# Kernel optimization log

Hardware: AMD Instinct MI355X
Metric: run time of the kernel (lower is better)

The kernel has to match this reference:

```python
import jax, jax.numpy as jnp
import numpy as np

T, M, K, B, H, L, V = 64, 256, 6, 256, 256, 128, 780
E = T * M
PAD = E  # padding slot in hidden buffer = Lorentz origin

def _to_lorentz_np(s):
    t = np.sqrt(1.0 + (s * s).sum(-1, keepdims=True))
    return np.concatenate([t, s], -1).astype(np.float32)

def setup_inputs() -> dict:
    rng = np.random.default_rng(0)
    def make_nei():
        idx = np.full((T, M, K), PAD, np.int64)
        w = np.zeros((T, M, K), np.float32)
        for t in range(T):
            deg = rng.integers(0, K + 1, size=M)
            if t == 0:
                deg[:] = 0  # no messages exist yet
            mask = np.arange(K)[None, :] < deg[:, None]
            cand = rng.integers(0, max(1, t * M), size=(M, K))  # only already-computed slots
            idx[t] = np.where(mask, cand, PAD)
            w[t] = mask.astype(np.float32)
            w[t, deg == 0, 0] = 1.0  # zero-neighbor case -> use origin padding (as in torch code)
        return idx.astype(np.int32), w
    nei_h_idx, nei_h_w = make_nei()
    nei_o_idx, nei_o_w = make_nei()
    return dict(
        wid=jnp.asarray(rng.integers(0, V, size=(T, M)), jnp.int32),
        nei_h_idx=jnp.asarray(nei_h_idx), nei_h_w=jnp.asarray(nei_h_w),
        nei_o_idx=jnp.asarray(nei_o_idx), nei_o_w=jnp.asarray(nei_o_w),
        batch_idx=jnp.asarray(rng.integers(0, B, size=(T, M)), jnp.int32),
        direction=jnp.asarray(rng.integers(0, 2, size=(T, M)), jnp.int32),
        pred_target=jnp.asarray(rng.integers(0, V, size=(T, M)), jnp.int32),
        root_wid=jnp.asarray(rng.integers(0, V, size=(B,)), jnp.int32),
        root_o_idx=jnp.asarray(rng.integers(0, E, size=(B, K)), jnp.int32),
        root_o_w=jnp.ones((B, K), jnp.float32),
        x_tree_vecs=jnp.asarray(_to_lorentz_np(rng.standard_normal((B, L - 1)) * 0.5)),
        embedding=jnp.asarray(_to_lorentz_np(rng.standard_normal((V, H - 1)) * 0.5)),
        W0=jnp.asarray(rng.standard_normal((H, H)) * 0.02, dtype=jnp.float32),
        b0=jnp.zeros((H,), jnp.float32),
        s0=jnp.asarray(np.log(10.0), jnp.float32),
        W1=jnp.asarray(rng.standard_normal((H, 2 * H - 1)) * 0.02, dtype=jnp.float32),
        b1=jnp.zeros((H,), jnp.float32),
        s1=jnp.asarray(np.log(10.0), jnp.float32),
        wcls=jnp.asarray(_to_lorentz_np(rng.standard_normal((V, H + L - 2)) * 0.5)),
        wbias=jnp.zeros((V,), jnp.float32),
        ucls=jnp.asarray(_to_lorentz_np(rng.standard_normal((2, 2 * H + L - 3)) * 0.5)),
        ubias=jnp.zeros((2,), jnp.float32),
    )

def _llinear(x, W, b, scale):
    # LorentzLinear: affine map, then rescale space part so output stays on the hyperboloid
    x = x @ W.T + b
    xs = x[..., 1:]
    time = jax.nn.sigmoid(x[..., :1]) * jnp.exp(scale) + 1.1
    sq = (time * time - 1.0) / jnp.clip((xs * xs).sum(-1, keepdims=True), 1e-8)
    return jnp.concatenate([time, xs * jnp.sqrt(sq)], -1)

def _mid_point(x, w):
    # Lorentz centroid: weighted mean renormalized to the manifold. x: [...,K,d], w: [...,K]
    ave = jnp.einsum('...k,...kd->...d', w, x) / jnp.clip(w.sum(-1, keepdims=True), 1e-8)
    inner = (ave[..., 1:] ** 2).sum(-1, keepdims=True) - ave[..., :1] ** 2  # <ave,ave>_L
    return ave / jnp.sqrt(jnp.clip(-inner, 1e-8))

def _concat(x, y):
    # hyperbolic concat: keep space parts, recompute time (dim = d1+d2-1)
    time = jnp.sqrt(jnp.clip(x[..., :1] ** 2 + y[..., :1] ** 2 - 1.0, 1e-8))
    return jnp.concatenate([time, x[..., 1:], y[..., 1:]], -1)

def _centroid(x, cls_pts, bias):
    # LorentzCentroidDistance logits: 2 + 2*<x, c>_L + bias
    inner = x[..., 1:] @ cls_pts[:, 1:].T - x[..., :1] * cls_pts[None, :, 0]
    return 2.0 + 2.0 * inner + bias

def _ce(scores, tgt):
    lp = jax.nn.log_softmax(scores, -1)
    return -jnp.take_along_axis(lp, tgt[:, None], axis=-1)[:, 0]

def _forward_core(wid, nei_h_idx, nei_h_w, nei_o_idx, nei_o_w, batch_idx, direction,
                  pred_target, root_wid, root_o_idx, root_o_w, x_tree_vecs, embedding,
                  W0, b0, s0, W1, b1, s1, wcls, wbias, ucls, ubias):
    hbuf0 = jnp.zeros((E + 1, H), jnp.float32).at[:, 0].set(1.0)  # all origin; slot E is padding

    def step(carry, xs_t):
        hbuf, t = carry
        wid_t, idx_t, w_t = xs_t
        cur_x = embedding[wid_t]                      # [M,H]
        h_nei = hbuf[idx_t]                           # [M,K,H] gather of prior messages
        h1 = _llinear(h_nei, W0, b0, s0)              # A0
        h1m = _mid_point(h1, w_t)                     # [M,H]
        new_h = _llinear(_concat(cur_x, h1m), W1, b1, s1)  # A1
        hbuf = jax.lax.dynamic_update_slice(hbuf, new_h, (t * M, 0))
        return (hbuf, t + jnp.int32(1)), new_h

    (hbuf, _), new_h = jax.lax.scan(step, (hbuf0, jnp.int32(0)), (wid, nei_h_idx, nei_h_w))
    new_h = new_h.reshape(E, H)
    cur_x = embedding[wid.reshape(E)]
    cur_o = _mid_point(hbuf[nei_o_idx.reshape(E, K)], nei_o_w.reshape(E, K))
    ctx = x_tree_vecs[batch_idx.reshape(E)]

    # word prediction: roots (origin hidden) + forward-direction messages
    origin = jnp.zeros((B, H), jnp.float32).at[:, 0].set(1.0)
    root_scores = _centroid(_concat(origin, x_tree_vecs), wcls, wbias)   # [B,V]
    msg_scores = _centroid(_concat(new_h, ctx), wcls, wbias)             # [E,V]
    pmask = direction.reshape(E).astype(jnp.float32)
    pt = pred_target.reshape(E)
    pred_loss = (_ce(root_scores, root_wid).sum() + (pmask * _ce(msg_scores, pt)).sum()) / B
    pred_hit = ((jnp.argmax(root_scores, -1) == root_wid).astype(jnp.float32).sum()
                + (pmask * (jnp.argmax(msg_scores, -1) == pt).astype(jnp.float32)).sum())
    pred_acc = pred_hit / (B + pmask.sum())

    # stop prediction: every message + final per-tree root entry (target 0)
    stop_h = _concat(_concat(cur_x, cur_o), ctx)                         # [E, 2H+L-2]
    root_o = _mid_point(hbuf[root_o_idx], root_o_w)
    stop_root = _concat(_concat(embedding[root_wid], root_o), x_tree_vecs)
    stop_scores = _centroid(jnp.concatenate([stop_h, stop_root], 0), ucls, ubias)
    stop_tgt = jnp.concatenate([direction.reshape(E), jnp.zeros((B,), jnp.int32)], 0)
    stop_loss = _ce(stop_scores, stop_tgt).sum() / B
    stop_acc = (jnp.argmax(stop_scores, -1) == stop_tgt).astype(jnp.float32).mean()
    return pred_loss, stop_loss, pred_acc, stop_acc

def reference(wid, nei_h_idx, nei_h_w, nei_o_idx, nei_o_w, batch_idx, direction,
              pred_target, root_wid, root_o_idx, root_o_w, x_tree_vecs, embedding,
              W0, b0, s0, W1, b1, s1, wcls, wbias, ucls, ubias):
    return _forward_core(wid, nei_h_idx, nei_h_w, nei_o_idx, nei_o_w, batch_idx, direction,
                         pred_target, root_wid, root_o_idx, root_o_w, x_tree_vecs, embedding,
                         W0, b0, s0, W1, b1, s1, wcls, wbias, ucls, ubias)
```

## Files before the change

### kernel.cpp

```cpp
#include <hip/hip_runtime.h>
#include <math.h>

#define T_ 64
#define M_ 256
#define K_ 6
#define B_ 256
#define H_ 256
#define L_ 128
#define V_ 780
#define E_ (T_*M_)
#define ZD 383
#define UD 638
#define KP 384
#define VP 832
#define TAG_PAD 0x7fffffffu

typedef unsigned short ushort_t;
typedef __attribute__((ext_vector_type(8))) _Float16 half8v;
typedef __attribute__((ext_vector_type(4))) _Float16 half4v;
typedef __attribute__((ext_vector_type(2))) _Float16 half2v;
typedef __attribute__((ext_vector_type(4))) float f32x4v;
typedef unsigned long long u64;


__device__ __forceinline__ float blk_sum(float v, float* red) {
    int j = threadIdx.x;
    #pragma unroll
    for (int o = 32; o > 0; o >>= 1) v += __shfl_down(v, o, 64);
    __syncthreads();
    if ((j & 63) == 0) red[j >> 6] = v;
    __syncthreads();
    return red[0] + red[1] + red[2] + red[3];
}

__device__ __forceinline__ float wave_sum(float v) {
    #pragma unroll
    for (int o = 32; o > 0; o >>= 1) v += __shfl_xor(v, o, 64);
    return v;
}

__device__ __forceinline__ _Float16 f2h(float x) { return (_Float16)x; }

__device__ __forceinline__ u64 llc_load8(const u64* p) {
    return __hip_atomic_load(p, __ATOMIC_RELAXED, __HIP_MEMORY_SCOPE_AGENT);
}
__device__ __forceinline__ void llc_store8(u64* p, u64 v) {
    __hip_atomic_store(p, v, __ATOMIC_RELAXED, __HIP_MEMORY_SCOPE_AGENT);
}


#define PREP_R0 ((E_ + 1) * H_)
#define PREP_RT ((E_ + 1) * 128)
#define PREP_R1 65536
#define PREP_R2 65536
#define PREP_R3 (VP * KP)
#define PREP_R4 65536
#define PREP_TOTAL (PREP_R0 + PREP_RT + PREP_R1 + PREP_R2 + PREP_R3 + PREP_R4)

__global__ __launch_bounds__(256) void prep_k(const float* __restrict__ W0,
                                              const float* __restrict__ W1,
                                              const float* __restrict__ wcls,
                                              float* __restrict__ hbuf,
                                              u64* __restrict__ hbuf2,
                                              _Float16* __restrict__ W0P,
                                              _Float16* __restrict__ W1HP,
                                              _Float16* __restrict__ Wh,
                                              float* __restrict__ W1T) {
    int idx = blockIdx.x * 256 + threadIdx.x;
    if (idx < PREP_R0) {
        hbuf[idx] = (idx >= E_ * H_ && (idx & (H_ - 1)) == 0) ? 1.f : 0.f;
        return;
    }
    idx -= PREP_R0;
    if (idx < PREP_RT) {
        int row = idx >> 7, cp = idx & 127;
        u64 val = 0ull;
        if (row == E_) {
            unsigned int lo = (cp == 0) ? 0x3C00u : 0u;
            val = ((u64)TAG_PAD << 32) | lo;
        }
        hbuf2[idx] = val;
        return;
    }
    idx -= PREP_RT;
    if (idx < PREP_R1) {
        int e = idx & 7, l = (idx >> 3) & 63, ks = (idx >> 9) & 7, nt = idx >> 12;
        int jj = nt * 16 + (l & 15);
        int ii = ks * 32 + (l >> 4) * 8 + e;
        W0P[idx] = f2h(W0[(size_t)jj * H_ + ii]);
        return;
    }
    idx -= PREP_R1;
    if (idx < PREP_R2) {
        int e = idx & 7, l = (idx >> 3) & 63, ks = (idx >> 9) & 7, nt = idx >> 12;
        int jj = nt * 16 + (l & 15);
        int ii = ks * 32 + (l >> 4) * 8 + e;
        float v = (ii == 0) ? W1[(size_t)jj * (2 * H_ - 1)]
                            : W1[(size_t)jj * (2 * H_ - 1) + 255 + ii];
        W1HP[idx] = f2h(v);
        return;
    }
    idx -= PREP_R2;
    if (idx < PREP_R3) {
        int v = idx / KP, k = idx - v * KP;
        float val = (v < V_ && k < ZD) ? wcls[(size_t)v * ZD + k] : 0.f;
        Wh[idx] = f2h(val);
        return;
    }
    idx -= PREP_R3;
    if (idx < PREP_R4) {
        int i = idx >> 8, j = idx & 255;
        W1T[idx] = (i >= 1) ? W1[(size_t)j * (2 * H_ - 1) + i] : 0.f;
    }
}


__global__ __launch_bounds__(256) void basew_k(const float* __restrict__ emb,
                                               const float* __restrict__ W1T,
                                               const float* __restrict__ b1,
                                               float* __restrict__ basew) {
    int v = blockIdx.x, j = threadIdx.x;
    __shared__ float cxs[256];
    cxs[j] = emb[(size_t)v * H_ + j];
    __syncthreads();
    float acc = b1[j];
    #pragma unroll 8
    for (int i = 1; i < 256; i++) acc = fmaf(cxs[i], W1T[i * 256 + j], acc);
    basew[(size_t)v * H_ + j] = acc;
}


__global__ __launch_bounds__(256, 1) void scan_flow(float* __restrict__ hbuf,
        u64* __restrict__ hbuf2,
        const _Float16* __restrict__ W0P, const float* __restrict__ b0, const float* __restrict__ s0p,
        const _Float16* __restrict__ W1HP, const float* __restrict__ s1p,
        const float* __restrict__ emb, const int* __restrict__ wid,
        const int* __restrict__ nhi, const float* __restrict__ nhw,
        const float* __restrict__ basew) {
    int tid = threadIdx.x;
    int w = tid >> 6, l = tid & 63;
    int quad = l >> 4, col = l & 15;
    int m = blockIdx.x;
    int j0 = 4 * l;

    __shared__ __align__(16) _Float16 hn16[16][264];
    __shared__ __align__(16) _Float16 zz16[264];
    __shared__ __align__(16) float Ys[6][256];
    __shared__ __align__(16) float y2s[256];

    half8v w0f[4][8], w1f[4][8];
    #pragma unroll
    for (int q = 0; q < 4; q++) {
        int nt = 4 * w + q;
        #pragma unroll
        for (int ks = 0; ks < 8; ks++) {
            w0f[q][ks] = *(const half8v*)(W0P + ((size_t)(nt * 8 + ks) * 64 + l) * 8);
            w1f[q][ks] = *(const half8v*)(W1HP + ((size_t)(nt * 8 + ks) * 64 + l) * 8);
        }
    }

    float es0 = expf(s0p[0]);
    float es1 = expf(s1p[0]);
    float4 bj4 = *(const float4*)(b0 + j0);
    int cp = tid & 127;
    int rsel = tid >> 7;

    for (int t = 0; t < T_; t++) {
        int e = t * M_ + m;
        const float* wp = nhw + e * K_;

        float wk[K_];
        #pragma unroll
        for (int k = 0; k < K_; k++) wk[k] = wp[k];
        int wde = wid[e];
        float4 bw4 = *(const float4*)(basew + (size_t)wde * H_ + j0);
        float cx0 = emb[(size_t)wde * H_];

        int nid[3];
        unsigned int tagx[3];
        const u64* pp[3];
        union { u64 u; unsigned int w2[2]; } pv[3];
        #pragma unroll
        for (int p = 0; p < 3; p++) {
            int row = 2 * p + rsel;
            int id = nhi[e * K_ + row];
            nid[p] = id;
            tagx[p] = (id < E_) ? (unsigned int)(id >> 8) + 1u : TAG_PAD;
            pp[p] = hbuf2 + ((size_t)id << 7) + cp;
            pv[p].u = llc_load8(pp[p]);
        }
        #pragma unroll
        for (int p = 0; p < 3; p++) {
            while (pv[p].w2[1] != tagx[p]) {
                __builtin_amdgcn_s_sleep(1);
                pv[p].u = llc_load8(pp[p]);
            }
            int row = 2 * p + rsel;
            *(unsigned int*)&hn16[row][cp * 2] = pv[p].w2[0];
        }
        __syncthreads();

        f32x4v acc[4];
        #pragma unroll
        for (int q = 0; q < 4; q++) acc[q] = (f32x4v){0.f, 0.f, 0.f, 0.f};
        #pragma unroll
        for (int ks = 0; ks < 8; ks++) {
            half8v afr = *(const half8v*)&hn16[col][ks * 32 + quad * 8];
            #pragma unroll
            for (int q = 0; q < 4; q++)
                acc[q] = __builtin_amdgcn_mfma_f32_16x16x32_f16(afr, w0f[q][ks], acc[q], 0, 0, 0);
        }
        #pragma unroll
        for (int q = 0; q < 4; q++) {
            int nt = 4 * w + q;
            #pragma unroll
            for (int r = 0; r < 4; r++) {
                int row = quad * 4 + r;
                if (row < 6) Ys[row][nt * 16 + col] = acc[q][r];
            }
        }
        __syncthreads();

        float y[K_][4];
        #pragma unroll
        for (int k = 0; k < K_; k++) {
            float4 yv = *(const float4*)&Ys[k][j0];
            y[k][0] = yv.x + bj4.x; y[k][1] = yv.y + bj4.y;
            y[k][2] = yv.z + bj4.z; y[k][3] = yv.w + bj4.w;
        }
        float c[K_];
        #pragma unroll
        for (int k = 0; k < K_; k++) {
            float cc = y[k][0] * y[k][0] + y[k][1] * y[k][1]
                     + y[k][2] * y[k][2] + y[k][3] * y[k][3];
            if (l == 0) cc -= y[k][0] * y[k][0];
            c[k] = cc;
        }
        #pragma unroll
        for (int o = 32; o > 0; o >>= 1) {
            #pragma unroll
            for (int k = 0; k < K_; k++) c[k] += __shfl_xor(c[k], o, 64);
        }
        float y0b[K_];
        #pragma unroll
        for (int k = 0; k < K_; k++) y0b[k] = __shfl(y[k][0], 0, 64);

        float ave[4] = {0.f, 0.f, 0.f, 0.f};
        float wsum = 0.f;
        #pragma unroll
        for (int k = 0; k < K_; k++) {
            float tm = es0 / (1.f + expf(-y0b[k])) + 1.1f;
            float sc = sqrtf((tm * tm - 1.f) / fmaxf(c[k], 1e-8f));
            #pragma unroll
            for (int c2 = 0; c2 < 4; c2++) {
                float h1v = (l == 0 && c2 == 0) ? tm : y[k][c2] * sc;
                ave[c2] += wk[k] * h1v;
            }
            wsum += wk[k];
        }
        float inv = 1.f / fmaxf(wsum, 1e-8f);
        float innl = 0.f;
        #pragma unroll
        for (int c2 = 0; c2 < 4; c2++) { ave[c2] *= inv; innl += ave[c2] * ave[c2]; }
        if (l == 0) innl -= 2.f * ave[0] * ave[0];
        float inner = wave_sum(innl);
        float rsc = 1.f / sqrtf(fmaxf(-inner, 1e-8f));

        if (w == 0) {
            #pragma unroll
            for (int c2 = 0; c2 < 4; c2++) {
                int j = j0 + c2;
                float h1m = ave[c2] * rsc;
                if (j == 0) {
                    zz16[0] = f2h(sqrtf(fmaxf(cx0 * cx0 + h1m * h1m - 1.f, 1e-8f)));
                } else {
                    zz16[j] = f2h(h1m);
                }
            }
        }
        __syncthreads();

        f32x4v a2[4];
        #pragma unroll
        for (int q = 0; q < 4; q++) a2[q] = (f32x4v){0.f, 0.f, 0.f, 0.f};
        #pragma unroll
        for (int ks = 0; ks < 8; ks++) {
            half8v zfr = *(const half8v*)&zz16[ks * 32 + quad * 8];
            #pragma unroll
            for (int q = 0; q < 4; q++)
                a2[q] = __builtin_amdgcn_mfma_f32_16x16x32_f16(zfr, w1f[q][ks], a2[q], 0, 0, 0);
        }
        if (quad == 0) {
            #pragma unroll
            for (int q = 0; q < 4; q++) y2s[(4 * w + q) * 16 + col] = a2[q][0];
        }
        __syncthreads();

        if (w == 0) {
            float4 y2v = *(const float4*)&y2s[j0];
            float y2[4] = {y2v.x + bw4.x, y2v.y + bw4.y, y2v.z + bw4.z, y2v.w + bw4.w};
            float c2s = y2[0] * y2[0] + y2[1] * y2[1] + y2[2] * y2[2] + y2[3] * y2[3];
            if (l == 0) c2s -= y2[0] * y2[0];
            float ssq2 = wave_sum(c2s);
            float y20 = __shfl(y2[0], 0, 64);
            float tm2 = es1 / (1.f + expf(-y20)) + 1.1f;
            float sc2 = sqrtf((tm2 * tm2 - 1.f) / fmaxf(ssq2, 1e-8f));
            float hv0 = (l == 0) ? tm2 : y2[0] * sc2;
            float hv1 = y2[1] * sc2, hv2 = y2[2] * sc2, hv3 = y2[3] * sc2;

            float4 out4 = {hv0, hv1, hv2, hv3};
            *(float4*)(hbuf + (size_t)e * H_ + j0) = out4;

            unsigned int tag = (unsigned int)t + 1u;
            union { half2v h; unsigned int u; } c01, c23;
            c01.h.x = f2h(hv0); c01.h.y = f2h(hv1);
            c23.h.x = f2h(hv2); c23.h.y = f2h(hv3);
            u64* pb = hbuf2 + ((size_t)e << 7) + 2 * l;
            llc_store8(pb,     ((u64)tag << 32) | c01.u);
            llc_store8(pb + 1, ((u64)tag << 32) | c23.u);
        }
    }
}


__global__ __launch_bounds__(256) void zbuild2(const float* __restrict__ hbuf,
                                               const float* __restrict__ xtv,
                                               const int* __restrict__ bidx,
                                               _Float16* __restrict__ Zh) {
    int e = blockIdx.x, j = threadIdx.x;
    int bi = bidx[e];
    _Float16* zr = Zh + (size_t)e * KP;
    if (j == 0) {
        float nh0 = hbuf[(size_t)e * H_];
        float c0  = xtv[(size_t)bi * L_];
        float z0  = sqrtf(fmaxf(nh0 * nh0 + c0 * c0 - 1.f, 1e-8f));
        zr[0] = f2h(-z0);
    } else {
        zr[j] = f2h(hbuf[(size_t)e * H_ + j]);
    }
    if (j < 128) {
        int c = 256 + j;
        float v = (c <= 382) ? xtv[(size_t)bi * L_ + (c - 255)] : 0.f;
        zr[c] = f2h(v);
    }
}


__global__ __launch_bounds__(256) void gemm_ce(const _Float16* __restrict__ Zh,
                                               const _Float16* __restrict__ Wh,
                                               const float* __restrict__ wbias,
                                               const int* __restrict__ pt,
                                               const int* __restrict__ dir,
                                               float* __restrict__ part) {
    __shared__ __align__(16) _Float16 As[64][392];
    __shared__ __align__(16) _Float16 Bsf[64][392];
    __shared__ __align__(16) float SCs[64][68];
    __shared__ float rmax[64], rsum[64], rval[64];
    __shared__ int   rargi[64];

    int tid = threadIdx.x;
    int w = tid >> 6, l = tid & 63;
    int r16 = l & 15, quad = l >> 4;
    int q8 = quad * 8;
    int m0 = blockIdx.x * 64;

    #pragma unroll
    for (int i = 0; i < 12; i++) {
        int u = tid + i * 256;
        int row = u / 48, c8 = (u % 48) * 8;
        *(uint4*)&As[row][c8] = *(const uint4*)(Zh + (size_t)(m0 + row) * KP + c8);
    }
    if (tid < 64) {
        rmax[tid] = -1e30f; rsum[tid] = 0.f; rargi[tid] = 0; rval[tid] = 0.f;
    }
    __syncthreads();

    for (int nt = 0; nt < 13; nt++) {
        int n0 = nt * 64;
        #pragma unroll
        for (int i = 0; i < 12; i++) {
            int u = tid + i * 256;
            int row = u / 48, c8 = (u % 48) * 8;
            *(uint4*)&Bsf[row][c8] = *(const uint4*)(Wh + (size_t)(n0 + row) * KP + c8);
        }
        __syncthreads();

        f32x4v acc[4];
        #pragma unroll
        for (int mt = 0; mt < 4; mt++) acc[mt] = (f32x4v){0.f, 0.f, 0.f, 0.f};
        #pragma unroll
        for (int ks = 0; ks < 12; ks++) {
            half8v bfr = *(const half8v*)&Bsf[w * 16 + r16][ks * 32 + q8];
            #pragma unroll
            for (int mt = 0; mt < 4; mt++) {
                half8v afr = *(const half8v*)&As[mt * 16 + r16][ks * 32 + q8];
                acc[mt] = __builtin_amdgcn_mfma_f32_16x16x32_f16(afr, bfr, acc[mt], 0, 0, 0);
            }
        }
        int ncol = n0 + w * 16 + r16;
        float bias = (ncol < V_) ? wbias[ncol] : 0.f;
        #pragma unroll
        for (int mt = 0; mt < 4; mt++) {
            #pragma unroll
            for (int r = 0; r < 4; r++)
                SCs[mt * 16 + quad * 4 + r][w * 16 + r16] = 2.f + 2.f * acc[mt][r] + bias;
        }
        __syncthreads();

        {
            int row = tid >> 2, prt = tid & 3;
            int tg = pt[m0 + row];
            float vals[16];
            float lm = -1e30f; int li = 0;
            #pragma unroll
            for (int c = 0; c < 16; c++) {
                int nc = n0 + prt * 16 + c;
                float x = (nc < V_) ? SCs[row][prt * 16 + c] : -1e30f;
                vals[c] = x;
                if (x > lm) { lm = x; li = nc; }
                if (nc == tg) rval[row] = x;
            }
            #pragma unroll
            for (int o = 1; o < 4; o <<= 1) {
                float om = __shfl_xor(lm, o, 64);
                int   oi = __shfl_xor(li, o, 64);
                if (om > lm || (om == lm && oi < li)) { lm = om; li = oi; }
            }
            float ls = 0.f;
            #pragma unroll
            for (int c = 0; c < 16; c++) {
                int nc = n0 + prt * 16 + c;
                if (nc < V_) ls += expf(vals[c] - lm);
            }
            #pragma unroll
            for (int o = 1; o < 4; o <<= 1) ls += __shfl_xor(ls, o, 64);
            if (prt == 0) {
                float om = rmax[row], os = rsum[row];
                float nm = fmaxf(om, lm);
                rsum[row] = os * expf(om - nm) + ls * expf(lm - nm);
                if (lm > om) rargi[row] = li;
                rmax[row] = nm;
            }
        }
        __syncthreads();
    }

    if (tid < 64) {
        int e = m0 + tid;
        int tg = pt[e];
        float pm = (float)dir[e];
        float lse = rmax[tid] + logf(rsum[tid]);
        float lloss = pm * (lse - rval[tid]);
        float lhit  = pm * ((rargi[tid] == tg) ? 1.f : 0.f);
        float lpm   = pm;
        lloss = wave_sum(lloss);
        lhit  = wave_sum(lhit);
        lpm   = wave_sum(lpm);
        if (tid == 0) {
            float* pr = part + (size_t)blockIdx.x * 8;
            pr[0] = lloss; pr[1] = lhit; pr[2] = lpm;
            pr[3] = 0.f; pr[4] = 0.f;
        }
    }
}


__global__ __launch_bounds__(256) void stoproot_k(const float* __restrict__ hbuf,
        const float* __restrict__ emb, const float* __restrict__ xtv,
        const int* __restrict__ wid, const int* __restrict__ noi, const float* __restrict__ now_w,
        const int* __restrict__ bidx, const int* __restrict__ dir,
        const int* __restrict__ rwid, const int* __restrict__ roi, const float* __restrict__ row_w,
        const float* __restrict__ wcls, const float* __restrict__ wbias,
        const float* __restrict__ ucls, const float* __restrict__ ubias,
        float* __restrict__ part) {
    __shared__ float red[256];
    __shared__ int   redi[256];
    __shared__ float shs[4];
    __shared__ float ctxs[L_];
    __shared__ float sc[V_];
    __shared__ float red2[4][2];

    if (blockIdx.x < 256) {
        int w = threadIdx.x >> 6, l = threadIdx.x & 63;
        int wg = blockIdx.x * 4 + w;

        float ua0[4], ub0[4], ua1[4], ub1[4], uc0[2], uc1[2];
        #pragma unroll
        for (int s = 0; s < 4; s++) {
            int j = s * 64 + l;
            ua0[s] = ucls[j];        ub0[s] = ucls[255 + j];
            ua1[s] = ucls[UD + j];   ub1[s] = ucls[UD + 255 + j];
        }
        #pragma unroll
        for (int s = 0; s < 2; s++) {
            int j = s * 64 + l;
            uc0[s] = ucls[510 + j];  uc1[s] = ucls[UD + 510 + j];
        }
        float u00 = ucls[0], u10 = ucls[UD];
        float ubs0 = ubias[0], ubs1 = ubias[1];

        float lloss = 0.f, lhit = 0.f;
        for (int i = 0; i < 16; i++) {
            int e = wg * 16 + i;
            const int*   ip = noi + e * K_;
            const float* wp = now_w + e * K_;
            float ave[4] = {0.f, 0.f, 0.f, 0.f};
            float wsum = 0.f;
            #pragma unroll
            for (int k = 0; k < K_; k++) {
                int id = ip[k]; float wt = wp[k];
                wsum += wt;
                const float* hr = hbuf + (size_t)id * H_;
                #pragma unroll
                for (int s = 0; s < 4; s++) ave[s] += wt * hr[s * 64 + l];
            }
            float inv = 1.f / fmaxf(wsum, 1e-8f);
            float innl = 0.f;
            #pragma unroll
            for (int s = 0; s < 4; s++) { ave[s] *= inv; innl += ave[s] * ave[s]; }
            if (l == 0) innl -= 2.f * ave[0] * ave[0];
            float inner = wave_sum(innl);
            float cs = 1.f / sqrtf(fmaxf(-inner, 1e-8f));

            int we = wid[e], bi = bidx[e];
            const float* er = emb + (size_t)we * H_;
            const float* cr = xtv + (size_t)bi * L_;

            float p0 = 0.f, p1 = 0.f;
            #pragma unroll
            for (int s = 0; s < 4; s++) {
                float cx = er[s * 64 + l];
                float co = ave[s] * cs;
                if (s == 0 && l == 0) {
                    float ctx0 = cr[0];
                    float t1sq = fmaxf(cx * cx + co * co - 1.f, 1e-8f);
                    float sh0 = sqrtf(fmaxf(t1sq + ctx0 * ctx0 - 1.f, 1e-8f));
                    p0 += -sh0 * u00; p1 += -sh0 * u10;
                } else {
                    p0 += cx * ua0[s] + co * ub0[s];
                    p1 += cx * ua1[s] + co * ub1[s];
                }
                if (s < 2) {
                    int j = s * 64 + l;
                    if (j >= 1) {
                        float ctx = cr[j];
                        p0 += ctx * uc0[s]; p1 += ctx * uc1[s];
                    }
                }
            }
            p0 = wave_sum(p0); p1 = wave_sum(p1);
            if (l == 0) {
                float sc0 = 2.f + 2.f * p0 + ubs0;
                float sc1 = 2.f + 2.f * p1 + ubs1;
                int tgt = dir[e];
                float mm = fmaxf(sc0, sc1);
                float lse = mm + logf(expf(sc0 - mm) + expf(sc1 - mm));
                lloss += lse - ((tgt == 0) ? sc0 : sc1);
                int am = (sc1 > sc0) ? 1 : 0;
                lhit += (am == tgt) ? 1.f : 0.f;
            }
        }
        if (l == 0) { red2[w][0] = lloss; red2[w][1] = lhit; }
        __syncthreads();
        if (threadIdx.x == 0) {
            float* pr = part + (size_t)(256 + blockIdx.x) * 8;
            pr[0] = 0.f; pr[1] = 0.f; pr[2] = 0.f;
            pr[3] = red2[0][0] + red2[1][0] + red2[2][0] + red2[3][0];
            pr[4] = red2[0][1] + red2[1][1] + red2[2][1] + red2[3][1];
        }
    } else {
        int b = blockIdx.x - 256, j = threadIdx.x;
        float* pr = part + (size_t)(512 + b) * 8;

        const int*   ip = roi + b * K_;
        const float* wp = row_w + b * K_;
        float ave = 0.f, wsum = 0.f;
        #pragma unroll
        for (int k = 0; k < K_; k++) {
            int id = ip[k]; float w = wp[k];
            ave += w * hbuf[(size_t)id * H_ + j];
            wsum += w;
        }
        ave /= fmaxf(wsum, 1e-8f);
        float inner = blk_sum((j == 0) ? -ave * ave : ave * ave, red);
        float ro = ave / sqrtf(fmaxf(-inner, 1e-8f));

        int   rw = rwid[b];
        float er = emb[(size_t)rw * H_ + j];
        float ctxj = (j < L_) ? xtv[(size_t)b * L_ + j] : 0.f;
        if (j == 0) { shs[0] = er; shs[1] = ro; shs[2] = ctxj; }
        if (j < L_) ctxs[j] = ctxj;
        __syncthreads();
        float t1sq = fmaxf(shs[0] * shs[0] + shs[1] * shs[1] - 1.f, 1e-8f);
        float sh0  = sqrtf(fmaxf(t1sq + shs[2] * shs[2] - 1.f, 1e-8f));

        float p0, p1;
        if (j >= 1) {
            p0 = er * ucls[j] + ro * ucls[255 + j];
            p1 = er * ucls[UD + j] + ro * ucls[UD + 255 + j];
            if (j < L_) { p0 += ctxj * ucls[510 + j]; p1 += ctxj * ucls[UD + 510 + j]; }
        } else {
            p0 = -sh0 * ucls[0];
            p1 = -sh0 * ucls[UD];
        }
        float s0 = 2.f + 2.f * blk_sum(p0, red) + ubias[0];
        float s1 = 2.f + 2.f * blk_sum(p1, red) + ubias[1];
        if (j == 0) {
            float mm = fmaxf(s0, s1);
            float lse = mm + logf(expf(s0 - mm) + expf(s1 - mm));
            int am = (s1 > s0) ? 1 : 0;
            pr[3] = lse - s0;
            pr[4] = (am == 0) ? 1.f : 0.f;
        }

        float c0 = shs[2];
        float z0 = sqrtf(fmaxf(c0 * c0, 1e-8f));
        __syncthreads();
        for (int v = j; v < V_; v += 256) {
            const float* wv = wcls + (size_t)v * ZD;
            float d = -z0 * wv[0];
            for (int i = 1; i < L_; i++) d += ctxs[i] * wv[255 + i];
            sc[v] = 2.f + 2.f * d + wbias[v];
        }
        __syncthreads();
        float mx = -1e30f; int mi = 0;
        for (int v = j; v < V_; v += 256) { float x = sc[v]; if (x > mx) { mx = x; mi = v; } }
        red[j] = mx; redi[j] = mi;
        __syncthreads();
        for (int o = 128; o > 0; o >>= 1) {
            if (j < o) {
                float xo = red[j + o]; int io = redi[j + o];
                if (xo > red[j] || (xo == red[j] && io < redi[j])) { red[j] = xo; redi[j] = io; }
            }
            __syncthreads();
        }
        float gm = red[0]; int ga = redi[0];
        __syncthreads();
        float se = 0.f;
        for (int v = j; v < V_; v += 256) se += expf(sc[v] - gm);
        red[j] = se;
        __syncthreads();
        for (int o = 128; o > 0; o >>= 1) { if (j < o) red[j] += red[j + o]; __syncthreads(); }
        if (j == 0) {
            float lse = gm + logf(red[0]);
            pr[0] = lse - sc[rw];
            pr[1] = (ga == rw) ? 1.f : 0.f;
            pr[2] = 0.f;
        }
    }
}


__global__ __launch_bounds__(256) void finalize2(const float* __restrict__ part,
                                                 float* __restrict__ out) {
    int j = threadIdx.x;
    __shared__ float red[256][5];
    #pragma unroll
    for (int c = 0; c < 5; c++)
        red[j][c] = part[(size_t)j * 8 + c] + part[(size_t)(j + 256) * 8 + c]
                  + part[(size_t)(j + 512) * 8 + c];
    __syncthreads();
    for (int o = 128; o > 0; o >>= 1) {
        if (j < o) {
            #pragma unroll
            for (int c = 0; c < 5; c++) red[j][c] += red[j + o][c];
        }
        __syncthreads();
    }
    if (j == 0) {
        out[0] = red[0][0] / (float)B_;
        out[1] = red[0][3] / (float)B_;
        out[2] = red[0][1] / ((float)B_ + red[0][2]);
        out[3] = red[0][4] / (float)(E_ + B_);
    }
}


extern "C" void kernel_launch(void* const* d_in, const int* in_sizes, int n_in,
                              void* d_out, int out_size, void* d_ws, size_t ws_size,
                              hipStream_t stream) {
    const int*   wid   = (const int*)d_in[0];
    const int*   nhi   = (const int*)d_in[1];
    const float* nhw   = (const float*)d_in[2];
    const int*   noi   = (const int*)d_in[3];
    const float* now_w = (const float*)d_in[4];
    const int*   bidx  = (const int*)d_in[5];
    const int*   dir   = (const int*)d_in[6];
    const int*   pt    = (const int*)d_in[7];
    const int*   rwid  = (const int*)d_in[8];
    const int*   roi   = (const int*)d_in[9];
    const float* row_w = (const float*)d_in[10];
    const float* xtv   = (const float*)d_in[11];
    const float* emb   = (const float*)d_in[12];
    const float* W0    = (const float*)d_in[13];
    const float* b0    = (const float*)d_in[14];
    const float* s0    = (const float*)d_in[15];
    const float* W1    = (const float*)d_in[16];
    const float* b1    = (const float*)d_in[17];
    const float* s1    = (const float*)d_in[18];
    const float* wcls  = (const float*)d_in[19];
    const float* wbias = (const float*)d_in[20];
    const float* ucls  = (const float*)d_in[21];
    const float* ubias = (const float*)d_in[22];

    float* ws    = (float*)d_ws;
    float* hbuf  = ws;
    u64*   hbuf2 = (u64*)(hbuf + (size_t)(E_ + 1) * H_);
    float* part  = (float*)(hbuf2 + (size_t)(E_ + 1) * 128);
    float* basew = part + 768 * 8;
    float* W1T   = basew + (size_t)V_ * H_;
    _Float16* W0P  = (_Float16*)(W1T + 65536);
    _Float16* W1HP = W0P + 65536;
    _Float16* Zh   = W1HP + 65536;
    _Float16* Wh   = Zh + (size_t)E_ * KP;
    float* out  = (float*)d_out;

    prep_k<<<(PREP_TOTAL + 255) / 256, 256, 0, stream>>>(W0, W1, wcls, hbuf, hbuf2,
                                                         W0P, W1HP, Wh, W1T);
    basew_k<<<V_, 256, 0, stream>>>(emb, W1T, b1, basew);

    scan_flow<<<M_, 256, 0, stream>>>(hbuf, hbuf2, W0P, b0, s0, W1HP, s1,
                                      emb, wid, nhi, nhw, basew);

    zbuild2<<<E_, 256, 0, stream>>>(hbuf, xtv, bidx, Zh);
    gemm_ce<<<256, 256, 0, stream>>>(Zh, Wh, wbias, pt, dir, part);
    stoproot_k<<<512, 256, 0, stream>>>(hbuf, emb, xtv, wid, noi, now_w, bidx, dir,
                                        rwid, roi, row_w, wcls, wbias, ucls, ubias, part);
    finalize2<<<1, 256, 0, stream>>>(part, out);
}
```

Baseline: 583.8 us.

## Prefetch neighbor rows directly into MFMA A-fragments and drop block barriers

The sequential scan kernel now loads each step's neighbor hidden rows straight into per-lane registers laid out as MFMA A-fragments. The loads for the next timestep are issued before the current step's math, so fetch latency overlaps compute, and the LDS staging buffer and its barrier are removed. Each wave also computes its own copy of the z vector in private shared memory, which removes another __syncthreads. The fp32 hbuf store is moved after the tagged publish stores so dependent blocks see results sooner. The cost is many extra registers (32 u64 prefetch values per lane) and redundant z computation in every wave.

```diff
diff --git a/kernel.cpp b/kernel.cpp
--- a/kernel.cpp
+++ b/kernel.cpp
@@ -142,9 +142,10 @@
     int quad = l >> 4, col = l & 15;
     int m = blockIdx.x;
     int j0 = 4 * l;
-
-    __shared__ __align__(16) _Float16 hn16[16][264];
-    __shared__ __align__(16) _Float16 zz16[264];
+    int r = col;
+    bool act = (r < K_);
+
+    __shared__ __align__(16) _Float16 zzs[4][264];
     __shared__ __align__(16) float Ys[6][256];
     __shared__ __align__(16) float y2s[256];
 
@@ -162,8 +163,23 @@
     float es0 = expf(s0p[0]);
     float es1 = expf(s1p[0]);
     float4 bj4 = *(const float4*)(b0 + j0);
-    int cp = tid & 127;
-    int rsel = tid >> 7;
+
+    unsigned int tagc = TAG_PAD;
+    const u64* rpc = hbuf2 + ((size_t)E_ << 7);
+    u64 pv[8][4];
+    {
+        int id = E_;
+        if (act) id = nhi[(size_t)m * K_ + r];
+        tagc = (id < E_) ? (unsigned int)(id >> 8) + 1u : TAG_PAD;
+        rpc = hbuf2 + ((size_t)id << 7);
+        if (act) {
+            #pragma unroll
+            for (int ks = 0; ks < 8; ks++)
+                #pragma unroll
+                for (int c = 0; c < 4; c++)
+                    pv[ks][c] = llc_load8(rpc + ks * 16 + quad * 4 + c);
+        }
+    }
 
     for (int t = 0; t < T_; t++) {
         int e = t * M_ + m;
@@ -176,47 +192,60 @@
         float4 bw4 = *(const float4*)(basew + (size_t)wde * H_ + j0);
         float cx0 = emb[(size_t)wde * H_];
 
-        int nid[3];
-        unsigned int tagx[3];
-        const u64* pp[3];
-        union { u64 u; unsigned int w2[2]; } pv[3];
-        #pragma unroll
-        for (int p = 0; p < 3; p++) {
-            int row = 2 * p + rsel;
-            int id = nhi[e * K_ + row];
-            nid[p] = id;
-            tagx[p] = (id < E_) ? (unsigned int)(id >> 8) + 1u : TAG_PAD;
-            pp[p] = hbuf2 + ((size_t)id << 7) + cp;
-            pv[p].u = llc_load8(pp[p]);
-        }
-        #pragma unroll
-        for (int p = 0; p < 3; p++) {
-            while (pv[p].w2[1] != tagx[p]) {
-                __builtin_amdgcn_s_sleep(1);
-                pv[p].u = llc_load8(pp[p]);
-            }
-            int row = 2 * p + rsel;
-            *(unsigned int*)&hn16[row][cp * 2] = pv[p].w2[0];
-        }
-        __syncthreads();
+        if (act) {
+            #pragma unroll
+            for (int ks = 0; ks < 8; ks++) {
+                #pragma unroll
+                for (int c = 0; c < 4; c++) {
+                    while ((unsigned int)(pv[ks][c] >> 32) != tagc) {
+                        __builtin_amdgcn_s_sleep(1);
+                        pv[ks][c] = llc_load8(rpc + ks * 16 + quad * 4 + c);
+                    }
+                }
+            }
+        }
+        half8v af[8];
+        #pragma unroll
+        for (int ks = 0; ks < 8; ks++) {
+            union { half8v h; unsigned int u[4]; u64 q[2]; } cv;
+            if (act) {
+                #pragma unroll
+                for (int c = 0; c < 4; c++) cv.u[c] = (unsigned int)pv[ks][c];
+            } else {
+                cv.q[0] = 0ull; cv.q[1] = 0ull;
+            }
+            af[ks] = cv.h;
+        }
+        if (t + 1 < T_) {
+            int id2 = E_;
+            if (act) id2 = nhi[(size_t)(e + M_) * K_ + r];
+            tagc = (id2 < E_) ? (unsigned int)(id2 >> 8) + 1u : TAG_PAD;
+            rpc = hbuf2 + ((size_t)id2 << 7);
+            if (act) {
+                #pragma unroll
+                for (int ks = 0; ks < 8; ks++)
+                    #pragma unroll
+                    for (int c = 0; c < 4; c++)
+                        pv[ks][c] = llc_load8(rpc + ks * 16 + quad * 4 + c);
+            }
+        }
 
         f32x4v acc[4];
         #pragma unroll
         for (int q = 0; q < 4; q++) acc[q] = (f32x4v){0.f, 0.f, 0.f, 0.f};
         #pragma unroll
         for (int ks = 0; ks < 8; ks++) {
-            half8v afr = *(const half8v*)&hn16[col][ks * 32 + quad * 8];
             #pragma unroll
             for (int q = 0; q < 4; q++)
-                acc[q] = __builtin_amdgcn_mfma_f32_16x16x32_f16(afr, w0f[q][ks], acc[q], 0, 0, 0);
+                acc[q] = __builtin_amdgcn_mfma_f32_16x16x32_f16(af[ks], w0f[q][ks], acc[q], 0, 0, 0);
         }
         #pragma unroll
         for (int q = 0; q < 4; q++) {
             int nt = 4 * w + q;
             #pragma unroll
-            for (int r = 0; r < 4; r++) {
-                int row = quad * 4 + r;
-                if (row < 6) Ys[row][nt * 16 + col] = acc[q][r];
+            for (int rr = 0; rr < 4; rr++) {
+                int row = quad * 4 + rr;
+                if (row < 6) Ys[row][nt * 16 + col] = acc[q][rr];
             }
         }
         __syncthreads();
@@ -266,26 +295,23 @@
         float inner = wave_sum(innl);
         float rsc = 1.f / sqrtf(fmaxf(-inner, 1e-8f));
 
-        if (w == 0) {
-            #pragma unroll
-            for (int c2 = 0; c2 < 4; c2++) {
-                int j = j0 + c2;
-                float h1m = ave[c2] * rsc;
-                if (j == 0) {
-                    zz16[0] = f2h(sqrtf(fmaxf(cx0 * cx0 + h1m * h1m - 1.f, 1e-8f)));
-                } else {
-                    zz16[j] = f2h(h1m);
-                }
-            }
-        }
-        __syncthreads();
+        #pragma unroll
+        for (int c2 = 0; c2 < 4; c2++) {
+            int j = j0 + c2;
+            float h1m = ave[c2] * rsc;
+            if (j == 0) {
+                zzs[w][0] = f2h(sqrtf(fmaxf(cx0 * cx0 + h1m * h1m - 1.f, 1e-8f)));
+            } else {
+                zzs[w][j] = f2h(h1m);
+            }
+        }
 
         f32x4v a2[4];
         #pragma unroll
         for (int q = 0; q < 4; q++) a2[q] = (f32x4v){0.f, 0.f, 0.f, 0.f};
         #pragma unroll
         for (int ks = 0; ks < 8; ks++) {
-            half8v zfr = *(const half8v*)&zz16[ks * 32 + quad * 8];
+            half8v zfr = *(const half8v*)&zzs[w][ks * 32 + quad * 8];
             #pragma unroll
             for (int q = 0; q < 4; q++)
                 a2[q] = __builtin_amdgcn_mfma_f32_16x16x32_f16(zfr, w1f[q][ks], a2[q], 0, 0, 0);
@@ -308,9 +334,6 @@
             float hv0 = (l == 0) ? tm2 : y2[0] * sc2;
             float hv1 = y2[1] * sc2, hv2 = y2[2] * sc2, hv3 = y2[3] * sc2;
 
-            float4 out4 = {hv0, hv1, hv2, hv3};
-            *(float4*)(hbuf + (size_t)e * H_ + j0) = out4;
-
             unsigned int tag = (unsigned int)t + 1u;
             union { half2v h; unsigned int u; } c01, c23;
             c01.h.x = f2h(hv0); c01.h.y = f2h(hv1);
@@ -318,6 +341,9 @@
             u64* pb = hbuf2 + ((size_t)e << 7) + 2 * l;
             llc_store8(pb,     ((u64)tag << 32) | c01.u);
             llc_store8(pb + 1, ((u64)tag << 32) | c23.u);
+
+            float4 out4 = {hv0, hv1, hv2, hv3};
+            *(float4*)(hbuf + (size_t)e * H_ + j0) = out4;
         }
     }
 }
@@ -402,8 +428,8 @@
         #pragma unroll
         for (int mt = 0; mt < 4; mt++) {
             #pragma unroll
-            for (int r = 0; r < 4; r++)
-                SCs[mt * 16 + quad * 4 + r][w * 16 + r16] = 2.f + 2.f * acc[mt][r] + bias;
+            for (int rr = 0; rr < 4; rr++)
+                SCs[mt * 16 + quad * 4 + rr][w * 16 + r16] = 2.f + 2.f * acc[mt][rr] + bias;
         }
         __syncthreads();
 
```

Result: slower. 752.6 us (+28.9%).

## Prefetch next-step neighbor loads and drop a barrier in the scan kernel

Applied to the files above, without the earlier changes.

The sequential scan kernel now issues the tagged neighbor loads for step t+1 right after the current step's neighbors are consumed, so the L2 round trip overlaps the current step's compute. It also has every wave compute its own copy of the intermediate z vector in a per-wave shared buffer, which removes one block-wide barrier per step. The tagged fp16 store is moved ahead of the fp32 hbuf store so dependent blocks see it sooner. The trade-off is more redundant work per wave, plus prefetched values that may be stale and then need re-polling.

```diff
diff --git a/kernel.cpp b/kernel.cpp
--- a/kernel.cpp
+++ b/kernel.cpp
@@ -142,9 +142,11 @@
     int quad = l >> 4, col = l & 15;
     int m = blockIdx.x;
     int j0 = 4 * l;
+    int cp = tid & 127;
+    int rsel = tid >> 7;
 
     __shared__ __align__(16) _Float16 hn16[16][264];
-    __shared__ __align__(16) _Float16 zz16[264];
+    __shared__ __align__(16) _Float16 zzs[4][264];
     __shared__ __align__(16) float Ys[6][256];
     __shared__ __align__(16) float y2s[256];
 
@@ -162,8 +164,18 @@
     float es0 = expf(s0p[0]);
     float es1 = expf(s1p[0]);
     float4 bj4 = *(const float4*)(b0 + j0);
-    int cp = tid & 127;
-    int rsel = tid >> 7;
+
+    unsigned int tagx[3];
+    const u64* pp[3];
+    u64 pvv[3];
+    #pragma unroll
+    for (int p = 0; p < 3; p++) {
+        int row = 2 * p + rsel;
+        int id = nhi[(size_t)m * K_ + row];
+        tagx[p] = (id < E_) ? (unsigned int)(id >> 8) + 1u : TAG_PAD;
+        pp[p] = hbuf2 + ((size_t)id << 7) + cp;
+        pvv[p] = llc_load8(pp[p]);
+    }
 
     for (int t = 0; t < T_; t++) {
         int e = t * M_ + m;
@@ -176,29 +188,31 @@
         float4 bw4 = *(const float4*)(basew + (size_t)wde * H_ + j0);
         float cx0 = emb[(size_t)wde * H_];
 
-        int nid[3];
-        unsigned int tagx[3];
-        const u64* pp[3];
-        union { u64 u; unsigned int w2[2]; } pv[3];
-        #pragma unroll
-        for (int p = 0; p < 3; p++) {
-            int row = 2 * p + rsel;
-            int id = nhi[e * K_ + row];
-            nid[p] = id;
-            tagx[p] = (id < E_) ? (unsigned int)(id >> 8) + 1u : TAG_PAD;
-            pp[p] = hbuf2 + ((size_t)id << 7) + cp;
-            pv[p].u = llc_load8(pp[p]);
-        }
-        #pragma unroll
-        for (int p = 0; p < 3; p++) {
-            while (pv[p].w2[1] != tagx[p]) {
-                __builtin_amdgcn_s_sleep(1);
-                pv[p].u = llc_load8(pp[p]);
-            }
-            int row = 2 * p + rsel;
-            *(unsigned int*)&hn16[row][cp * 2] = pv[p].w2[0];
-        }
-        __syncthreads();
+        for (;;) {
+            bool ok = ((unsigned int)(pvv[0] >> 32) == tagx[0])
+                   && ((unsigned int)(pvv[1] >> 32) == tagx[1])
+                   && ((unsigned int)(pvv[2] >> 32) == tagx[2]);
+            if (ok) break;
+            __builtin_amdgcn_s_sleep(1);
+            #pragma unroll
+            for (int p = 0; p < 3; p++)
+                if ((unsigned int)(pvv[p] >> 32) != tagx[p]) pvv[p] = llc_load8(pp[p]);
+        }
+        #pragma unroll
+        for (int p = 0; p < 3; p++)
+            *(unsigned int*)&hn16[2 * p + rsel][cp * 2] = (unsigned int)pvv[p];
+        __syncthreads();
+
+        if (t + 1 < T_) {
+            #pragma unroll
+            for (int p = 0; p < 3; p++) {
+                int row = 2 * p + rsel;
+                int id = nhi[(size_t)(e + M_) * K_ + row];
+                tagx[p] = (id < E_) ? (unsigned int)(id >> 8) + 1u : TAG_PAD;
+                pp[p] = hbuf2 + ((size_t)id << 7) + cp;
+                pvv[p] = llc_load8(pp[p]);
+            }
+        }
 
         f32x4v acc[4];
         #pragma unroll
@@ -214,9 +228,9 @@
         for (int q = 0; q < 4; q++) {
             int nt = 4 * w + q;
             #pragma unroll
-            for (int r = 0; r < 4; r++) {
-                int row = quad * 4 + r;
-                if (row < 6) Ys[row][nt * 16 + col] = acc[q][r];
+            for (int rr = 0; rr < 4; rr++) {
+                int row = quad * 4 + rr;
+                if (row < 6) Ys[row][nt * 16 + col] = acc[q][rr];
             }
         }
         __syncthreads();
@@ -266,26 +280,23 @@
         float inner = wave_sum(innl);
         float rsc = 1.f / sqrtf(fmaxf(-inner, 1e-8f));
 
-        if (w == 0) {
-            #pragma unroll
-            for (int c2 = 0; c2 < 4; c2++) {
-                int j = j0 + c2;
-                float h1m = ave[c2] * rsc;
-                if (j == 0) {
-                    zz16[0] = f2h(sqrtf(fmaxf(cx0 * cx0 + h1m * h1m - 1.f, 1e-8f)));
-                } else {
-                    zz16[j] = f2h(h1m);
-                }
-            }
-        }
-        __syncthreads();
+        #pragma unroll
+        for (int c2 = 0; c2 < 4; c2++) {
+            int j = j0 + c2;
+            float h1m = ave[c2] * rsc;
+            if (j == 0) {
+                zzs[w][0] = f2h(sqrtf(fmaxf(cx0 * cx0 + h1m * h1m - 1.f, 1e-8f)));
+            } else {
+                zzs[w][j] = f2h(h1m);
+            }
+        }
 
         f32x4v a2[4];
         #pragma unroll
         for (int q = 0; q < 4; q++) a2[q] = (f32x4v){0.f, 0.f, 0.f, 0.f};
         #pragma unroll
         for (int ks = 0; ks < 8; ks++) {
-            half8v zfr = *(const half8v*)&zz16[ks * 32 + quad * 8];
+            half8v zfr = *(const half8v*)&zzs[w][ks * 32 + quad * 8];
             #pragma unroll
             for (int q = 0; q < 4; q++)
                 a2[q] = __builtin_amdgcn_mfma_f32_16x16x32_f16(zfr, w1f[q][ks], a2[q], 0, 0, 0);
@@ -308,9 +319,6 @@
             float hv0 = (l == 0) ? tm2 : y2[0] * sc2;
             float hv1 = y2[1] * sc2, hv2 = y2[2] * sc2, hv3 = y2[3] * sc2;
 
-            float4 out4 = {hv0, hv1, hv2, hv3};
-            *(float4*)(hbuf + (size_t)e * H_ + j0) = out4;
-
             unsigned int tag = (unsigned int)t + 1u;
             union { half2v h; unsigned int u; } c01, c23;
             c01.h.x = f2h(hv0); c01.h.y = f2h(hv1);
@@ -318,6 +326,9 @@
             u64* pb = hbuf2 + ((size_t)e << 7) + 2 * l;
             llc_store8(pb,     ((u64)tag << 32) | c01.u);
             llc_store8(pb + 1, ((u64)tag << 32) | c23.u);
+
+            float4 out4 = {hv0, hv1, hv2, hv3};
+            *(float4*)(hbuf + (size_t)e * H_ + j0) = out4;
         }
     }
 }
@@ -402,8 +413,8 @@
         #pragma unroll
         for (int mt = 0; mt < 4; mt++) {
             #pragma unroll
-            for (int r = 0; r < 4; r++)
-                SCs[mt * 16 + quad * 4 + r][w * 16 + r16] = 2.f + 2.f * acc[mt][r] + bias;
+            for (int rr = 0; rr < 4; rr++)
+                SCs[mt * 16 + quad * 4 + rr][w * 16 + r16] = 2.f + 2.f * acc[mt][rr] + bias;
         }
         __syncthreads();
 
```

After: 589.5 us. Within noise of the previous version (+1.0%).
